# Kernel tuning notes

Measured on AMD Instinct MI355X. Metric: run time of the kernel, lower is better.

## Reference

```python
import jax, jax.numpy as jnp
import numpy as np
from jax import lax

EPS = 1e-5
ODE_T1 = 6.0      # ODEnet uses timestep=6
ODE_NSTEPS = 12   # fixed-step RK4 replacing scipy LSODA


def _gn(x, groups, w, b):
    # GroupNorm over (C//groups, H, W) per group, affine per-channel
    N, C, H, W = x.shape
    xg = x.reshape(N, groups, -1)
    mu = xg.mean(-1, keepdims=True)
    var = xg.var(-1, keepdims=True)
    xn = ((xg - mu) * lax.rsqrt(var + EPS)).reshape(N, C, H, W)
    return xn * w[None, :, None, None] + b[None, :, None, None]


def _conv(x, w, stride=1, pad=1):
    return lax.conv_general_dilated(
        x, w, (stride, stride), [(pad, pad), (pad, pad)],
        dimension_numbers=('NCHW', 'OIHW', 'NCHW'))


def _residual(x, g1w, g1b, c1w, g2w, g2b, c2w, dw):
    # Residual block with stride-2 conv and 1x1 stride-2 downsample applied
    # to relu(norm1(x)) (exactly as in the torch code).
    h = jax.nn.relu(_gn(x, 32, g1w, g1b))
    skip = _conv(h, dw, stride=2, pad=0)
    h = _conv(h, c1w, stride=2, pad=1)
    h = jax.nn.relu(_gn(h, 32, g2w, g2b))
    h = _conv(h, c2w)
    return h + skip


def _odefunc(z, p):
    # ResidualODE.odefunc: GroupNorm with groups == channels (64)
    g1w, g1b, c1w, g2w, g2b, c2w = p
    h = jax.nn.relu(_gn(z, 64, g1w, g1b))
    h = _conv(h, c1w)
    h = jax.nn.relu(_gn(h, 64, g2w, g2b))
    h = _conv(h, c2w)
    return h + z


def _odeint_rk4(z0, p):
    dt = ODE_T1 / ODE_NSTEPS
    def step(z, _):
        k1 = _odefunc(z, p)
        k2 = _odefunc(z + 0.5 * dt * k1, p)
        k3 = _odefunc(z + 0.5 * dt * k2, p)
        k4 = _odefunc(z + dt * k3, p)
        return z + (dt / 6.0) * (k1 + 2.0 * k2 + 2.0 * k3 + k4), None
    z, _ = lax.scan(step, z0, None, length=ODE_NSTEPS)
    return z


def _forward(x, conv1_w, conv1_b,
             r1_g1w, r1_g1b, r1_c1w, r1_g2w, r1_g2b, r1_c2w, r1_dw,
             r2_g1w, r2_g1b, r2_c1w, r2_g2w, r2_g2b, r2_c2w, r2_dw,
             ode_g1w, ode_g1b, ode_c1w, ode_g2w, ode_g2b, ode_c2w,
             fin_gw, fin_gb, fc_w, fc_b):
    out = _conv(x, conv1_w, stride=1, pad=0) + conv1_b[None, :, None, None]  # (B,64,26,26)
    out = _residual(out, r1_g1w, r1_g1b, r1_c1w, r1_g2w, r1_g2b, r1_c2w, r1_dw)  # (B,64,13,13)
    out = _residual(out, r2_g1w, r2_g1b, r2_c1w, r2_g2w, r2_g2b, r2_c2w, r2_dw)  # (B,64,7,7)
    out = _odeint_rk4(out, (ode_g1w, ode_g1b, ode_c1w, ode_g2w, ode_g2b, ode_c2w))
    out = jax.nn.relu(_gn(out, 32, fin_gw, fin_gb))
    out = out.mean(axis=(2, 3))  # AdaptiveAvgPool2d((1,1)) + flatten -> (B,64)
    return out @ fc_w.T + fc_b   # (B,10)


def setup_inputs() -> dict:
    key = jax.random.key(0)
    ks = iter(jax.random.split(key, 16))
    n = lambda shape, s: jax.random.normal(next(ks), shape, dtype=jnp.float32) * s
    C = 64
    s3 = 0.05  # ~ kaiming std for 64x3x3 fan-in
    inp = {
        'x': n((512, 1, 28, 28), 1.0),
        'conv1_w': n((C, 1, 3, 3), 0.3),
        'conv1_b': jnp.zeros((C,), jnp.float32),
        'r1_g1w': jnp.ones((C,), jnp.float32), 'r1_g1b': jnp.zeros((C,), jnp.float32),
        'r1_c1w': n((C, C, 3, 3), s3),
        'r1_g2w': jnp.ones((C,), jnp.float32), 'r1_g2b': jnp.zeros((C,), jnp.float32),
        'r1_c2w': n((C, C, 3, 3), s3),
        'r1_dw': n((C, C, 1, 1), 0.12),
        'r2_g1w': jnp.ones((C,), jnp.float32), 'r2_g1b': jnp.zeros((C,), jnp.float32),
        'r2_c1w': n((C, C, 3, 3), s3),
        'r2_g2w': jnp.ones((C,), jnp.float32), 'r2_g2b': jnp.zeros((C,), jnp.float32),
        'r2_c2w': n((C, C, 3, 3), s3),
        'r2_dw': n((C, C, 1, 1), 0.12),
        'ode_g1w': jnp.ones((C,), jnp.float32), 'ode_g1b': jnp.zeros((C,), jnp.float32),
        'ode_c1w': n((C, C, 3, 3), s3),
        'ode_g2w': jnp.ones((C,), jnp.float32), 'ode_g2b': jnp.zeros((C,), jnp.float32),
        'ode_c2w': n((C, C, 3, 3), s3),
        'fin_gw': jnp.ones((C,), jnp.float32), 'fin_gb': jnp.zeros((C,), jnp.float32),
        'fc_w': n((10, C), 0.1),
        'fc_b': jnp.zeros((10,), jnp.float32),
    }
    return inp


def reference(x, conv1_w, conv1_b,
              r1_g1w, r1_g1b, r1_c1w, r1_g2w, r1_g2b, r1_c2w, r1_dw,
              r2_g1w, r2_g1b, r2_c1w, r2_g2w, r2_g2b, r2_c2w, r2_dw,
              ode_g1w, ode_g1b, ode_c1w, ode_g2w, ode_g2b, ode_c2w,
              fin_gw, fin_gb, fc_w, fc_b):
    return _forward(x, conv1_w, conv1_b,
                    r1_g1w, r1_g1b, r1_c1w, r1_g2w, r1_g2b, r1_c2w, r1_dw,
                    r2_g1w, r2_g1b, r2_c1w, r2_g2w, r2_g2b, r2_c2w, r2_dw,
                    ode_g1w, ode_g1b, ode_c1w, ode_g2w, ode_g2b, ode_c2w,
                    fin_gw, fin_gb, fc_w, fc_b)
```

## Files before the change

### kernel.cpp

```cpp
#include <hip/hip_runtime.h>
#include <hip/hip_bf16.h>

#define TPB 256

typedef __attribute__((ext_vector_type(8))) short short8;
typedef __attribute__((ext_vector_type(4))) float f32x4;

__device__ __forceinline__ unsigned short f2bf(float x) {
    union { float f; unsigned int u; } c; c.f = x;
    unsigned int u = c.u;
    unsigned int r = (u + 0x7fffu + ((u >> 16) & 1u)) >> 16;
    return (unsigned short)r;
}

#define IN_STATS(Xp, HW)                                                        \
    {                                                                           \
        int ch_ = t >> 2, sg_ = t & 3;                                          \
        float s_ = 0.f, s2_ = 0.f;                                              \
        for (int i_ = sg_; i_ < (HW); i_ += 4) {                                \
            float v_ = (Xp)[(size_t)ch_ * (HW) + i_];                           \
            s_ += v_; s2_ += v_ * v_;                                           \
        }                                                                       \
        rsum[t] = s_; rssq[t] = s2_;                                            \
        __syncthreads();                                                        \
        if (t < 32) {                                                           \
            float S = 0.f, S2 = 0.f;                                            \
            _Pragma("unroll")                                                   \
            for (int k_ = 0; k_ < 8; k_++) {                                    \
                int tt_ = (2 * t + (k_ & 1)) * 4 + (k_ >> 1);                   \
                S += rsum[tt_]; S2 += rssq[tt_];                                \
            }                                                                   \
            float mu_ = S / (2.f * (HW));                                       \
            sM[t] = mu_;                                                        \
            sR[t] = rsqrtf(S2 / (2.f * (HW)) - mu_ * mu_ + 1e-5f);              \
        }                                                                       \
        __syncthreads();                                                        \
    }


__global__ void conv1_k(const float* __restrict__ x, const float* __restrict__ w,
                        const float* __restrict__ b, float* __restrict__ out) {
    int idx = blockIdx.x * TPB + threadIdx.x;
    const int total = 512 * 64 * 26 * 26;
    if (idx >= total) return;
    int ox = idx % 26; int t = idx / 26;
    int oy = t % 26;   t /= 26;
    int co = t % 64;   int n = t / 64;
    const float* xp = x + (size_t)n * 784 + oy * 28 + ox;
    const float* wp = w + co * 9;
    float s = b[co];
#pragma unroll
    for (int ky = 0; ky < 3; ky++)
#pragma unroll
        for (int kx = 0; kx < 3; kx++)
            s += xp[ky * 28 + kx] * wp[ky * 3 + kx];
    out[idx] = s;
}


__global__ void gn_stats_k(const float* __restrict__ x, float* __restrict__ mean,
                           float* __restrict__ rstd, int N, int C, int HW, int G) {
    int gid  = (blockIdx.x * blockDim.x + threadIdx.x) >> 6;
    int lane = threadIdx.x & 63;
    int total = N * G;
    if (gid >= total) return;
    int n = gid / G, g = gid % G;
    int cpg = C / G;
    int gsize = cpg * HW;
    const float* p = x + ((size_t)n * C + (size_t)g * cpg) * HW;
    float s = 0.f, s2 = 0.f;
    for (int i = lane; i < gsize; i += 64) { float v = p[i]; s += v; s2 += v * v; }
#pragma unroll
    for (int off = 32; off; off >>= 1) {
        s  += __shfl_down(s,  off);
        s2 += __shfl_down(s2, off);
    }
    if (lane == 0) {
        float m = s / gsize;
        float var = s2 / gsize - m * m;
        mean[gid] = m;
        rstd[gid] = rsqrtf(var + 1e-5f);
    }
}


__global__ void wsplit_all_k(const float* __restrict__ w0, const float* __restrict__ w1,
                             const float* __restrict__ w2, const float* __restrict__ w3,
                             const float* __restrict__ w4, const float* __restrict__ w5,
                             const float* __restrict__ d0, const float* __restrict__ d1,
                             unsigned short* __restrict__ dst) {
    const int WBS = 9 * 2 * 4 * 64 * 8, WBS1 = 2 * 4 * 64 * 8;
    int i = blockIdx.x * TPB + threadIdx.x;
    if (i < 6 * WBS) {
        int tbl = i / WBS; int r = i - tbl * WBS;
        const float* w = (tbl == 0) ? w0 : (tbl == 1) ? w1 : (tbl == 2) ? w2
                       : (tbl == 3) ? w3 : (tbl == 4) ? w4 : w5;
        int j = r & 7, l = (r >> 3) & 63, nt = (r >> 9) & 3, ks = (r >> 11) & 1, tt = r >> 12;
        int co = nt * 16 + (l & 15);
        int ci = ks * 32 + (l >> 4) * 8 + j;
        dst[i] = f2bf(w[(co * 64 + ci) * 9 + tt]);
    } else {
        int r = i - 6 * WBS;
        if (r >= 2 * WBS1) return;
        int tbl = r / WBS1; r -= tbl * WBS1;
        const float* w = tbl ? d1 : d0;
        int j = r & 7, l = (r >> 3) & 63, nt = (r >> 9) & 3, ks = (r >> 11) & 1;
        int co = nt * 16 + (l & 15);
        int ci = ks * 32 + (l >> 4) * 8 + j;
        dst[6 * WBS + tbl * WBS1 + r] = f2bf(w[co * 64 + ci]);
    }
}


template<bool SELF>
__global__ __launch_bounds__(256, 2)
void conv_s2_mfma_k(const float* __restrict__ in,
                    const unsigned short* __restrict__ bhT,
                    const unsigned short* __restrict__ dwT,
                    float* __restrict__ out, float* __restrict__ skipout,
                    const float* __restrict__ mean, const float* __restrict__ rstd,
                    const float* __restrict__ gnw, const float* __restrict__ gnb,
                    int H, int W, int OH, int OW, int TX, int TY) {
    __shared__ unsigned short hp[256 * 72];
    __shared__ float rsum[256], rssq[256], sM[32], sR[32];

    int b = blockIdx.x;
    int tx = b % TX; b /= TX;
    int ty = b % TY; int n = b / TY;
    int oy0 = ty * 7, ox0 = tx * 7;

    const int t = threadIdx.x;
    const int lane = t & 63, nt = t >> 6;
    const int colL = lane & 15, q = lane >> 4;
    const int co = nt * 16 + colL;
    const int kq0 = q * 8;

    short8 wr[18], dr[2];
#pragma unroll
    for (int i = 0; i < 18; i++) wr[i] = ((const short8*)bhT)[(i * 4 + nt) * 64 + lane];
    dr[0] = ((const short8*)dwT)[(0 * 4 + nt) * 64 + lane];
    dr[1] = ((const short8*)dwT)[(1 * 4 + nt) * 64 + lane];

    for (int i = t; i < 256 * 72 / 2; i += 256) ((unsigned int*)hp)[i] = 0u;

    const float* ip = in + (size_t)n * 64 * H * W;
    if constexpr (SELF) {
        IN_STATS(ip, H * W)
    } else {
        if (t < 32) { sM[t] = mean[n * 32 + t]; sR[t] = rstd[n * 32 + t]; }
        __syncthreads();
    }

    for (int i = t; i < 64 * 240; i += 256) {
        int ch = i / 240; int rc = i - ch * 240;
        int r = rc >> 4, c = rc & 15;
        int iy = 2 * oy0 - 1 + r;
        int ix = (c < 8) ? (2 * ox0 + 2 * c) : (2 * ox0 - 1 + 2 * (c - 8));
        if ((unsigned)iy < (unsigned)H && (unsigned)ix < (unsigned)W) {
            float m = sM[ch >> 1], rs = sR[ch >> 1];
            float raw = ip[(size_t)ch * H * W + iy * W + ix];
            float v = fmaxf((raw - m) * rs * gnw[ch] + gnb[ch], 0.f);
            hp[(r * 16 + c) * 72 + ch] = f2bf(v);
        }
    }
    __syncthreads();

    int bs0, bs1, bs2, bs3;
    {
#define BSLOT(dst, mm)                                                          \
        {                                                                       \
            int p_ = (mm) * 16 + colL;                                          \
            int oy_ = p_ >> 3, ox_ = p_ & 7;                                    \
            dst = (ox_ < 7 && oy_ < 7) ? ((2 * oy_) * 16 + ox_) : 0;            \
        }
        BSLOT(bs0, 0) BSLOT(bs1, 1) BSLOT(bs2, 2) BSLOT(bs3, 3)
#undef BSLOT
    }

    f32x4 a0, a1, a2, a3, k0, k1, k2, k3;
    a0 = (f32x4){0.f, 0.f, 0.f, 0.f}; a1 = a0; a2 = a0; a3 = a0;
    k0 = a0; k1 = a0; k2 = a0; k3 = a0;

#pragma unroll
    for (int t9 = 0; t9 < 9; t9++) {
        const int kx = t9 % 3;
        const int toff = (t9 / 3) * 16 + (kx == 0 ? 8 : (kx == 1 ? 0 : 9));
#pragma unroll
        for (int ks = 0; ks < 2; ks++) {
            short8 vb = wr[t9 * 2 + ks];
            int kq = ks * 32 + kq0;
#define TAP(areg, bs)                                                           \
            {                                                                   \
                short8 av = *(const short8*)(hp + ((bs) + toff) * 72 + kq);     \
                areg = __builtin_amdgcn_mfma_f32_16x16x32_bf16(av, vb, areg, 0, 0, 0); \
            }
            TAP(a0, bs0) TAP(a1, bs1) TAP(a2, bs2) TAP(a3, bs3)
#undef TAP
        }
    }
#pragma unroll
    for (int ks = 0; ks < 2; ks++) {
        short8 vb = dr[ks];
        int kq = ks * 32 + kq0;
#define TAP(areg, bs)                                                           \
        {                                                                       \
            short8 av = *(const short8*)(hp + ((bs) + 16) * 72 + kq);           \
            areg = __builtin_amdgcn_mfma_f32_16x16x32_bf16(av, vb, areg, 0, 0, 0); \
        }
        TAP(k0, bs0) TAP(k1, bs1) TAP(k2, bs2) TAP(k3, bs3)
#undef TAP
    }

#define WB(areg, kreg, mm)                                                      \
    _Pragma("unroll")                                                           \
    for (int j = 0; j < 4; j++) {                                               \
        int p_ = (mm) * 16 + q * 4 + j;                                         \
        int oy_ = p_ >> 3, ox_ = p_ & 7;                                        \
        if (ox_ < 7 && oy_ < 7 && oy0 + oy_ < OH && ox0 + ox_ < OW) {           \
            size_t idx = (((size_t)n * 64 + co) * OH + oy0 + oy_) * OW + ox0 + ox_; \
            out[idx] = areg[j];                                                 \
            skipout[idx] = kreg[j];                                             \
        }                                                                       \
    }
    WB(a0, k0, 0) WB(a1, k1, 1) WB(a2, k2, 2) WB(a3, k3, 3)
#undef WB
}


__global__ __launch_bounds__(256, 2)
void conv13_mfma_k(const float* __restrict__ in, const unsigned short* __restrict__ bhT,
                   float* __restrict__ io,
                   const float* __restrict__ gnw, const float* __restrict__ gnb) {
    __shared__ unsigned short hp[256 * 72];
    __shared__ float rsum[256], rssq[256], sM[32], sR[32];
    const int t = threadIdx.x;
    const int n = blockIdx.x;
    const int lane = t & 63;
    const int nt = t >> 6;
    const int colL = lane & 15, q = lane >> 4;
    const int co = nt * 16 + colL;
    const int kq0 = q * 8;

    short8 wr[18];
#pragma unroll
    for (int i = 0; i < 18; i++) wr[i] = ((const short8*)bhT)[(i * 4 + nt) * 64 + lane];

    for (int i = t; i < 256 * 72 / 2; i += 256) ((unsigned int*)hp)[i] = 0u;

    const float* ip = in + (size_t)n * 64 * 169;
    IN_STATS(ip, 169)

    for (int i = t; i < 64 * 169; i += 256) {
        int ch = i / 169, p = i - ch * 169;
        int y = p / 13, x = p - y * 13;
        float m = sM[ch >> 1], rs = sR[ch >> 1];
        float v = fmaxf((ip[i] - m) * rs * gnw[ch] + gnb[ch], 0.f);
        hp[((y + 1) * 16 + (x + 1)) * 72 + ch] = f2bf(v);
    }
    __syncthreads();

    int hb[11];
#pragma unroll
    for (int m = 0; m < 11; m++) {
        int p = m * 16 + colL;
        int y = p / 13, x = p - y * 13;
        hb[m] = (y + 1) * 16 + (x + 1);
    }
    f32x4 acc[11];
#pragma unroll
    for (int m = 0; m < 11; m++) acc[m] = (f32x4){0.f, 0.f, 0.f, 0.f};

#pragma unroll
    for (int t9 = 0; t9 < 9; t9++) {
        const int toff = (t9 / 3) * 16 + (t9 % 3) - 17;
#pragma unroll
        for (int ks = 0; ks < 2; ks++) {
            short8 vb = wr[t9 * 2 + ks];
            int kq = ks * 32 + kq0;
#pragma unroll
            for (int m = 0; m < 11; m++) {
                short8 a_ = *(const short8*)(hp + (hb[m] + toff) * 72 + kq);
                acc[m] = __builtin_amdgcn_mfma_f32_16x16x32_bf16(a_, vb, acc[m], 0, 0, 0);
            }
        }
    }

    float* op = io + (size_t)n * 64 * 169 + (size_t)co * 169;
#pragma unroll
    for (int m = 0; m < 11; m++) {
        int p0 = m * 16 + q * 4;
#pragma unroll
        for (int j = 0; j < 4; j++) {
            int p = p0 + j;
            if (p < 169) op[p] += acc[m][j];
        }
    }
}


#define HP_PITCH 72
#define HP_PLANE (100 * HP_PITCH)

#define PVALID(p) ((((p) & 7) < 7) && (((p) >> 3) < 7))
#define PSLOT(p)  (((((p) >> 3) + 1) * 10) + (((p) & 7) + 1))

#define CONV_TAP(areg, hbase)                                                   \
    {                                                                           \
        short8 a_ = *(const short8*)(hp + ((hbase) + toff) * HP_PITCH + kq);    \
        areg = __builtin_amdgcn_mfma_f32_16x16x32_bf16(a_, vb, areg, 0, 0, 0);  \
    }

#define CONV_MFMA(hpsrc, wreg)                                                  \
    a0 = (f32x4){0.f, 0.f, 0.f, 0.f}; a1 = a0; a2 = a0; a3 = a0;                \
    {                                                                           \
        const unsigned short* hp = (hpsrc);                                     \
        _Pragma("unroll")                                                       \
        for (int t9 = 0; t9 < 9; t9++) {                                        \
            const int toff = (t9 / 3) * 10 + (t9 % 3) - 11;                     \
            _Pragma("unroll")                                                   \
            for (int ks = 0; ks < 2; ks++) {                                    \
                short8 vb = wreg[t9 * 2 + ks];                                  \
                int kq = ks * 32 + kq0;                                         \
                CONV_TAP(a0, h0)                                                \
                CONV_TAP(a1, h1)                                                \
                CONV_TAP(a2, h2)                                                \
                CONV_TAP(a3, h3)                                                \
            }                                                                   \
        }                                                                       \
    }

#define CONV_MFMA_G(hpsrc, bhT)                                                 \
    a0 = (f32x4){0.f, 0.f, 0.f, 0.f}; a1 = a0; a2 = a0; a3 = a0;                \
    {                                                                           \
        const unsigned short* hp = (hpsrc);                                     \
        const short8* bh_ = (const short8*)(bhT);                               \
        _Pragma("unroll")                                                       \
        for (int t9 = 0; t9 < 9; t9++) {                                        \
            const int toff = (t9 / 3) * 10 + (t9 % 3) - 11;                     \
            _Pragma("unroll")                                                   \
            for (int ks = 0; ks < 2; ks++) {                                    \
                short8 vb = bh_[((t9 * 2 + ks) * 4 + nt) * 64 + lane];          \
                int kq = ks * 32 + kq0;                                         \
                CONV_TAP(a0, h0)                                                \
                CONV_TAP(a1, h1)                                                \
                CONV_TAP(a2, h2)                                                \
                CONV_TAP(a3, h3)                                                \
            }                                                                   \
        }                                                                       \
    }

#define GN_ACCUM(areg, mm)                                                      \
    _Pragma("unroll")                                                           \
    for (int j = 0; j < 4; j++) {                                               \
        int p_ = (mm) * 16 + q * 4 + j;                                         \
        if (PVALID(p_)) { float x_ = areg[j]; s += x_; s2 += x_ * x_; }         \
    }

#define GN_STORE(dst, areg, mm)                                                 \
    _Pragma("unroll")                                                           \
    for (int j = 0; j < 4; j++) {                                               \
        int p_ = (mm) * 16 + q * 4 + j;                                         \
        if (PVALID(p_)) {                                                       \
            float y_ = fmaxf(areg[j] * sc + sh, 0.f);                           \
            (dst)[PSLOT(p_) * HP_PITCH + co] = f2bf(y_);                        \
        }                                                                       \
    }

#define RK4_REG(areg, zm, zam, um)                                              \
    {                                                                           \
        f32x4 kv = areg + um;                                                   \
        zam = (e == 0) ? (zm + ck * kv) : (zam + ck * kv);                      \
        if (e < 3) um = zm + cu * kv;                                           \
    }

__global__ __launch_bounds__(256, 2)
void ode_mfma_k(const float* __restrict__ u7raw, const float* __restrict__ z7,
                const float* __restrict__ pgw, const float* __restrict__ pgb,
                const unsigned short* __restrict__ wr2h,
                const unsigned short* __restrict__ wb1h,
                const unsigned short* __restrict__ wb2h,
                const float* __restrict__ g1w, const float* __restrict__ g1b,
                const float* __restrict__ g2w, const float* __restrict__ g2b,
                const float* __restrict__ fgw, const float* __restrict__ fgb,
                const float* __restrict__ fcw, const float* __restrict__ fcb,
                float* __restrict__ out) {
    __shared__ unsigned short hp1[HP_PLANE], hp2[HP_PLANE];
    __shared__ float rsum[256], rssq[256], sM[32], sR[32];
    __shared__ float pooled[64];

    const int t = threadIdx.x;
    const int n = blockIdx.x;
    const int lane = t & 63;
    const int nt = t >> 6;
    const int colL = lane & 15, q = lane >> 4;
    const int co = nt * 16 + colL;

    const float g1wv = g1w[co], g1bv = g1b[co];
    const float g2wv = g2w[co], g2bv = g2b[co];

    const int h0 = PSLOT(colL);
    const int h1 = PSLOT(16 + colL);
    const int h2 = PSLOT(32 + colL);
    const int h3 = PSLOT(48 + colL);
    const int kq0 = q * 8;

    short8 w1r[18], w2r[18];
#pragma unroll
    for (int i = 0; i < 18; i++) {
        int fidx = (i * 4 + nt) * 64 + lane;
        w1r[i] = ((const short8*)wb1h)[fidx];
        w2r[i] = ((const short8*)wb2h)[fidx];
    }

    for (int i = t; i < HP_PLANE; i += 256) { hp1[i] = 0; hp2[i] = 0; }

    const float* up = u7raw + (size_t)n * 3136;
    IN_STATS(up, 49)

    for (int i = t; i < 3136; i += 256) {
        int ch = i / 49, r = i - ch * 49;
        int y = r / 7, x = r - y * 7;
        float m = sM[ch >> 1], rs = sR[ch >> 1];
        float v = fmaxf((up[i] - m) * rs * pgw[ch] + pgb[ch], 0.f);
        hp1[((y + 1) * 10 + (x + 1)) * HP_PITCH + ch] = f2bf(v);
    }
    __syncthreads();

    f32x4 zr0, zr1, zr2, zr3;
    f32x4 za0, za1, za2, za3;
    f32x4 ur0, ur1, ur2, ur3;
    {
        f32x4 a0, a1, a2, a3;
        CONV_MFMA_G(hp1, wr2h)
        const float* zb = z7 + (size_t)n * 3136 + (size_t)co * 49;
#define INITZ(zm, areg, mm)                                                     \
        _Pragma("unroll")                                                       \
        for (int j = 0; j < 4; j++) {                                           \
            int p_ = (mm) * 16 + q * 4 + j;                                     \
            zm[j] = PVALID(p_) ? (areg[j] + zb[(p_ >> 3) * 7 + (p_ & 7)]) : 0.f;\
        }
        INITZ(zr0, a0, 0) INITZ(zr1, a1, 1) INITZ(zr2, a2, 2) INITZ(zr3, a3, 3)
#undef INITZ
    }
    ur0 = zr0; ur1 = zr1; ur2 = zr2; ur3 = zr3;
    __syncthreads();

    const float dt = 0.5f;

#pragma unroll 1
    for (int step = 0; step < 12; step++) {
#pragma unroll 1
        for (int e = 0; e < 4; e++) {
            const float ck = (e == 0 || e == 3) ? dt / 6.f : dt / 3.f;
            const float cu = (e == 2) ? dt : 0.5f * dt;

            {
                float s = 0.f, s2 = 0.f;
                GN_ACCUM(ur0, 0) GN_ACCUM(ur1, 1) GN_ACCUM(ur2, 2) GN_ACCUM(ur3, 3)
                s += __shfl_xor(s, 16); s2 += __shfl_xor(s2, 16);
                s += __shfl_xor(s, 32); s2 += __shfl_xor(s2, 32);
                float mu = s * (1.f / 49.f);
                float r = rsqrtf(s2 * (1.f / 49.f) - mu * mu + 1e-5f);
                float sc = r * g1wv, sh = g1bv - mu * sc;
                GN_STORE(hp1, ur0, 0) GN_STORE(hp1, ur1, 1)
                GN_STORE(hp1, ur2, 2) GN_STORE(hp1, ur3, 3)
            }
            __syncthreads();

            {
                f32x4 a0, a1, a2, a3;
                CONV_MFMA(hp1, w1r)

                float s = 0.f, s2 = 0.f;
                GN_ACCUM(a0, 0) GN_ACCUM(a1, 1) GN_ACCUM(a2, 2) GN_ACCUM(a3, 3)
                s += __shfl_xor(s, 16); s2 += __shfl_xor(s2, 16);
                s += __shfl_xor(s, 32); s2 += __shfl_xor(s2, 32);
                float mu = s * (1.f / 49.f);
                float r = rsqrtf(s2 * (1.f / 49.f) - mu * mu + 1e-5f);
                float sc = r * g2wv, sh = g2bv - mu * sc;
                GN_STORE(hp2, a0, 0) GN_STORE(hp2, a1, 1)
                GN_STORE(hp2, a2, 2) GN_STORE(hp2, a3, 3)
            }
            __syncthreads();

            {
                f32x4 a0, a1, a2, a3;
                CONV_MFMA(hp2, w2r)

                RK4_REG(a0, zr0, za0, ur0) RK4_REG(a1, zr1, za1, ur1)
                RK4_REG(a2, zr2, za2, ur2) RK4_REG(a3, zr3, za3, ur3)
                if (e == 3) {
                    zr0 = za0; zr1 = za1; zr2 = za2; zr3 = za3;
                    ur0 = zr0; ur1 = zr1; ur2 = zr2; ur3 = zr3;
                }
            }
        }
    }

    {
        float s = 0.f, s2 = 0.f;
        GN_ACCUM(zr0, 0) GN_ACCUM(zr1, 1) GN_ACCUM(zr2, 2) GN_ACCUM(zr3, 3)
        s += __shfl_xor(s, 16); s2 += __shfl_xor(s2, 16);
        s += __shfl_xor(s, 32); s2 += __shfl_xor(s2, 32);
        s += __shfl_xor(s, 1);  s2 += __shfl_xor(s2, 1);
        float mu = s * (1.f / 98.f);
        float r = rsqrtf(s2 * (1.f / 98.f) - mu * mu + 1e-5f);
        float sc = r * fgw[co], sh = fgb[co] - mu * sc;
        float ps = 0.f;
#pragma unroll
        for (int mm = 0; mm < 4; mm++) {
            f32x4 zz = (mm == 0) ? zr0 : (mm == 1) ? zr1 : (mm == 2) ? zr2 : zr3;
#pragma unroll
            for (int j = 0; j < 4; j++) {
                int p_ = mm * 16 + q * 4 + j;
                if (PVALID(p_)) ps += fmaxf(zz[j] * sc + sh, 0.f);
            }
        }
        ps += __shfl_xor(ps, 16);
        ps += __shfl_xor(ps, 32);
        if (q == 0) pooled[co] = ps * (1.f / 49.f);
    }
    __syncthreads();
    if (t < 10) {
        float a = fcb[t];
#pragma unroll
        for (int k = 0; k < 64; k++) a += pooled[k] * fcw[t * 64 + k];
        out[(size_t)n * 10 + t] = a;
    }
}

static inline int nblk(long long total) { return (int)((total + TPB - 1) / TPB); }

extern "C" void kernel_launch(void* const* d_in, const int* in_sizes, int n_in,
                              void* d_out, int out_size, void* d_ws, size_t ws_size,
                              hipStream_t stream) {
    const float* x       = (const float*)d_in[0];
    const float* conv1_w = (const float*)d_in[1];
    const float* conv1_b = (const float*)d_in[2];
    const float* r1_g1w  = (const float*)d_in[3];
    const float* r1_g1b  = (const float*)d_in[4];
    const float* r1_c1w  = (const float*)d_in[5];
    const float* r1_g2w  = (const float*)d_in[6];
    const float* r1_g2b  = (const float*)d_in[7];
    const float* r1_c2w  = (const float*)d_in[8];
    const float* r1_dw   = (const float*)d_in[9];
    const float* r2_g1w  = (const float*)d_in[10];
    const float* r2_g1b  = (const float*)d_in[11];
    const float* r2_c1w  = (const float*)d_in[12];
    const float* r2_g2w  = (const float*)d_in[13];
    const float* r2_g2b  = (const float*)d_in[14];
    const float* r2_c2w  = (const float*)d_in[15];
    const float* r2_dw   = (const float*)d_in[16];
    const float* o_g1w   = (const float*)d_in[17];
    const float* o_g1b   = (const float*)d_in[18];
    const float* o_c1w   = (const float*)d_in[19];
    const float* o_g2w   = (const float*)d_in[20];
    const float* o_g2b   = (const float*)d_in[21];
    const float* o_c2w   = (const float*)d_in[22];
    const float* fin_gw  = (const float*)d_in[23];
    const float* fin_gb  = (const float*)d_in[24];
    const float* fc_w    = (const float*)d_in[25];
    const float* fc_b    = (const float*)d_in[26];
    float* out = (float*)d_out;

    const long long SZ26 = 512LL * 64 * 26 * 26;
    const long long SZ13 = 512LL * 64 * 13 * 13;
    const long long SZ7  = 512LL * 64 * 7 * 7;
    const long long WBS  = 9 * 2 * 4 * 64 * 8;
    const long long WBS1 = 2 * 4 * 64 * 8;

    float* B26   = (float*)d_ws;
    float* A13   = B26 + SZ26;
    float* B13   = A13 + SZ13;
    float* Z7    = B13 + SZ13;
    float* U7    = Z7 + SZ7;
    float* MEAN  = U7 + SZ7;
    float* RSTD  = MEAN + 512 * 32;
    unsigned short* WTAB  = (unsigned short*)(RSTD + 512 * 32);
    unsigned short* WB1h  = WTAB;
    unsigned short* WB2h  = WTAB + WBS;
    unsigned short* WB13h = WTAB + 2 * WBS;
    unsigned short* WR2h  = WTAB + 3 * WBS;
    unsigned short* WR11h = WTAB + 4 * WBS;
    unsigned short* WR21h = WTAB + 5 * WBS;
    unsigned short* WD1h  = WTAB + 6 * WBS;
    unsigned short* WD2h  = WTAB + 6 * WBS + WBS1;

    wsplit_all_k<<<nblk(6 * WBS + 2 * WBS1), TPB, 0, stream>>>(
        o_c1w, o_c2w, r1_c2w, r2_c2w, r1_c1w, r2_c1w, r1_dw, r2_dw, WTAB);

    conv1_k<<<nblk(SZ26), TPB, 0, stream>>>(x, conv1_w, conv1_b, B26);

    gn_stats_k<<<nblk(512LL * 32 * 64), TPB, 0, stream>>>(B26, MEAN, RSTD, 512, 64, 676, 32);
    conv_s2_mfma_k<false><<<512 * 4, 256, 0, stream>>>(B26, WR11h, WD1h, A13, B13,
                                                       MEAN, RSTD, r1_g1w, r1_g1b,
                                                       26, 26, 13, 13, 2, 2);
    conv13_mfma_k<<<512, 256, 0, stream>>>(A13, WB13h, B13, r1_g2w, r1_g2b);

    conv_s2_mfma_k<true><<<512, 256, 0, stream>>>(B13, WR21h, WD2h, U7, Z7,
                                                  nullptr, nullptr, r2_g1w, r2_g1b,
                                                  13, 13, 7, 7, 1, 1);

    ode_mfma_k<<<512, 256, 0, stream>>>(U7, Z7, r2_g2w, r2_g2b,
                                        WR2h, WB1h, WB2h,
                                        o_g1w, o_g1b, o_g2w, o_g2b,
                                        fin_gw, fin_gb, fc_w, fc_b, out);
}
```

Measured before the change: 607.5 us.

## Store inter-stage activations in bf16 and raise wave priority during MFMA loops

After: 581.6 us. -4.3%, faster.

```diff
diff --git a/kernel.cpp b/kernel.cpp
--- a/kernel.cpp
+++ b/kernel.cpp
@@ -12,13 +12,17 @@
     unsigned int r = (u + 0x7fffu + ((u >> 16) & 1u)) >> 16;
     return (unsigned short)r;
 }
-
-#define IN_STATS(Xp, HW)                                                        \
+__device__ __forceinline__ float bf2f(unsigned short h) {
+    union { unsigned int u; float f; } c; c.u = ((unsigned int)h) << 16;
+    return c.f;
+}
+
+#define IN_STATS_BF(Xp, HW)                                                     \
     {                                                                           \
         int ch_ = t >> 2, sg_ = t & 3;                                          \
         float s_ = 0.f, s2_ = 0.f;                                              \
         for (int i_ = sg_; i_ < (HW); i_ += 4) {                                \
-            float v_ = (Xp)[(size_t)ch_ * (HW) + i_];                           \
+            float v_ = bf2f((Xp)[(size_t)ch_ * (HW) + i_]);                     \
             s_ += v_; s2_ += v_ * v_;                                           \
         }                                                                       \
         rsum[t] = s_; rssq[t] = s2_;                                            \
@@ -39,7 +43,7 @@
 
 
 __global__ void conv1_k(const float* __restrict__ x, const float* __restrict__ w,
-                        const float* __restrict__ b, float* __restrict__ out) {
+                        const float* __restrict__ b, unsigned short* __restrict__ out) {
     int idx = blockIdx.x * TPB + threadIdx.x;
     const int total = 512 * 64 * 26 * 26;
     if (idx >= total) return;
@@ -54,12 +58,13 @@
 #pragma unroll
         for (int kx = 0; kx < 3; kx++)
             s += xp[ky * 28 + kx] * wp[ky * 3 + kx];
-    out[idx] = s;
-}
-
-
-__global__ void gn_stats_k(const float* __restrict__ x, float* __restrict__ mean,
-                           float* __restrict__ rstd, int N, int C, int HW, int G) {
+    out[idx] = f2bf(s);
+}
+
+
+__global__ void gn_stats_bf_k(const unsigned short* __restrict__ x,
+                              float* __restrict__ mean, float* __restrict__ rstd,
+                              int N, int C, int HW, int G) {
     int gid  = (blockIdx.x * blockDim.x + threadIdx.x) >> 6;
     int lane = threadIdx.x & 63;
     int total = N * G;
@@ -67,9 +72,9 @@
     int n = gid / G, g = gid % G;
     int cpg = C / G;
     int gsize = cpg * HW;
-    const float* p = x + ((size_t)n * C + (size_t)g * cpg) * HW;
+    const unsigned short* p = x + ((size_t)n * C + (size_t)g * cpg) * HW;
     float s = 0.f, s2 = 0.f;
-    for (int i = lane; i < gsize; i += 64) { float v = p[i]; s += v; s2 += v * v; }
+    for (int i = lane; i < gsize; i += 64) { float v = bf2f(p[i]); s += v; s2 += v * v; }
 #pragma unroll
     for (int off = 32; off; off >>= 1) {
         s  += __shfl_down(s,  off);
@@ -112,12 +117,12 @@
 }
 
 
-template<bool SELF>
+template<bool SELF, bool FP32SKIP>
 __global__ __launch_bounds__(256, 2)
-void conv_s2_mfma_k(const float* __restrict__ in,
+void conv_s2_mfma_k(const unsigned short* __restrict__ in,
                     const unsigned short* __restrict__ bhT,
                     const unsigned short* __restrict__ dwT,
-                    float* __restrict__ out, float* __restrict__ skipout,
+                    unsigned short* __restrict__ out, void* __restrict__ skipout_,
                     const float* __restrict__ mean, const float* __restrict__ rstd,
                     const float* __restrict__ gnw, const float* __restrict__ gnb,
                     int H, int W, int OH, int OW, int TX, int TY) {
@@ -143,9 +148,9 @@
 
     for (int i = t; i < 256 * 72 / 2; i += 256) ((unsigned int*)hp)[i] = 0u;
 
-    const float* ip = in + (size_t)n * 64 * H * W;
+    const unsigned short* ip = in + (size_t)n * 64 * H * W;
     if constexpr (SELF) {
-        IN_STATS(ip, H * W)
+        IN_STATS_BF(ip, H * W)
     } else {
         if (t < 32) { sM[t] = mean[n * 32 + t]; sR[t] = rstd[n * 32 + t]; }
         __syncthreads();
@@ -158,7 +163,7 @@
         int ix = (c < 8) ? (2 * ox0 + 2 * c) : (2 * ox0 - 1 + 2 * (c - 8));
         if ((unsigned)iy < (unsigned)H && (unsigned)ix < (unsigned)W) {
             float m = sM[ch >> 1], rs = sR[ch >> 1];
-            float raw = ip[(size_t)ch * H * W + iy * W + ix];
+            float raw = bf2f(ip[(size_t)ch * H * W + iy * W + ix]);
             float v = fmaxf((raw - m) * rs * gnw[ch] + gnb[ch], 0.f);
             hp[(r * 16 + c) * 72 + ch] = f2bf(v);
         }
@@ -218,8 +223,9 @@
         int oy_ = p_ >> 3, ox_ = p_ & 7;                                        \
         if (ox_ < 7 && oy_ < 7 && oy0 + oy_ < OH && ox0 + ox_ < OW) {           \
             size_t idx = (((size_t)n * 64 + co) * OH + oy0 + oy_) * OW + ox0 + ox_; \
-            out[idx] = areg[j];                                                 \
-            skipout[idx] = kreg[j];                                             \
+            out[idx] = f2bf(areg[j]);                                           \
+            if constexpr (FP32SKIP) ((float*)skipout_)[idx] = kreg[j];          \
+            else ((unsigned short*)skipout_)[idx] = f2bf(kreg[j]);              \
         }                                                                       \
     }
     WB(a0, k0, 0) WB(a1, k1, 1) WB(a2, k2, 2) WB(a3, k3, 3)
@@ -228,8 +234,9 @@
 
 
 __global__ __launch_bounds__(256, 2)
-void conv13_mfma_k(const float* __restrict__ in, const unsigned short* __restrict__ bhT,
-                   float* __restrict__ io,
+void conv13_mfma_k(const unsigned short* __restrict__ in,
+                   const unsigned short* __restrict__ bhT,
+                   unsigned short* __restrict__ io,
                    const float* __restrict__ gnw, const float* __restrict__ gnb) {
     __shared__ unsigned short hp[256 * 72];
     __shared__ float rsum[256], rssq[256], sM[32], sR[32];
@@ -247,14 +254,14 @@
 
     for (int i = t; i < 256 * 72 / 2; i += 256) ((unsigned int*)hp)[i] = 0u;
 
-    const float* ip = in + (size_t)n * 64 * 169;
-    IN_STATS(ip, 169)
+    const unsigned short* ip = in + (size_t)n * 64 * 169;
+    IN_STATS_BF(ip, 169)
 
     for (int i = t; i < 64 * 169; i += 256) {
         int ch = i / 169, p = i - ch * 169;
         int y = p / 13, x = p - y * 13;
         float m = sM[ch >> 1], rs = sR[ch >> 1];
-        float v = fmaxf((ip[i] - m) * rs * gnw[ch] + gnb[ch], 0.f);
+        float v = fmaxf((bf2f(ip[i]) - m) * rs * gnw[ch] + gnb[ch], 0.f);
         hp[((y + 1) * 16 + (x + 1)) * 72 + ch] = f2bf(v);
     }
     __syncthreads();
@@ -285,14 +292,14 @@
         }
     }
 
-    float* op = io + (size_t)n * 64 * 169 + (size_t)co * 169;
+    unsigned short* op = io + (size_t)n * 64 * 169 + (size_t)co * 169;
 #pragma unroll
     for (int m = 0; m < 11; m++) {
         int p0 = m * 16 + q * 4;
 #pragma unroll
         for (int j = 0; j < 4; j++) {
             int p = p0 + j;
-            if (p < 169) op[p] += acc[m][j];
+            if (p < 169) op[p] = f2bf(bf2f(op[p]) + acc[m][j]);
         }
     }
 }
@@ -314,6 +321,7 @@
     a0 = (f32x4){0.f, 0.f, 0.f, 0.f}; a1 = a0; a2 = a0; a3 = a0;                \
     {                                                                           \
         const unsigned short* hp = (hpsrc);                                     \
+        __builtin_amdgcn_s_setprio(1);                                          \
         _Pragma("unroll")                                                       \
         for (int t9 = 0; t9 < 9; t9++) {                                        \
             const int toff = (t9 / 3) * 10 + (t9 % 3) - 11;                     \
@@ -327,6 +335,7 @@
                 CONV_TAP(a3, h3)                                                \
             }                                                                   \
         }                                                                       \
+        __builtin_amdgcn_s_setprio(0);                                          \
     }
 
 #define CONV_MFMA_G(hpsrc, bhT)                                                 \
@@ -374,7 +383,7 @@
     }
 
 __global__ __launch_bounds__(256, 2)
-void ode_mfma_k(const float* __restrict__ u7raw, const float* __restrict__ z7,
+void ode_mfma_k(const unsigned short* __restrict__ u7raw, const float* __restrict__ z7,
                 const float* __restrict__ pgw, const float* __restrict__ pgb,
                 const unsigned short* __restrict__ wr2h,
                 const unsigned short* __restrict__ wb1h,
@@ -414,14 +423,14 @@
 
     for (int i = t; i < HP_PLANE; i += 256) { hp1[i] = 0; hp2[i] = 0; }
 
-    const float* up = u7raw + (size_t)n * 3136;
-    IN_STATS(up, 49)
+    const unsigned short* up = u7raw + (size_t)n * 3136;
+    IN_STATS_BF(up, 49)
 
     for (int i = t; i < 3136; i += 256) {
         int ch = i / 49, r = i - ch * 49;
         int y = r / 7, x = r - y * 7;
         float m = sM[ch >> 1], rs = sR[ch >> 1];
-        float v = fmaxf((up[i] - m) * rs * pgw[ch] + pgb[ch], 0.f);
+        float v = fmaxf((bf2f(up[i]) - m) * rs * pgw[ch] + pgb[ch], 0.f);
         hp1[((y + 1) * 10 + (x + 1)) * HP_PITCH + ch] = f2bf(v);
     }
     __syncthreads();
@@ -569,13 +578,13 @@
     const long long WBS  = 9 * 2 * 4 * 64 * 8;
     const long long WBS1 = 2 * 4 * 64 * 8;
 
-    float* B26   = (float*)d_ws;
-    float* A13   = B26 + SZ26;
-    float* B13   = A13 + SZ13;
-    float* Z7    = B13 + SZ13;
-    float* U7    = Z7 + SZ7;
-    float* MEAN  = U7 + SZ7;
-    float* RSTD  = MEAN + 512 * 32;
+    unsigned short* B26 = (unsigned short*)d_ws;
+    unsigned short* A13 = B26 + SZ26;
+    unsigned short* B13 = A13 + SZ13;
+    unsigned short* U7  = B13 + SZ13;
+    float* Z7   = (float*)(U7 + SZ7 + (SZ7 & 1));
+    float* MEAN = Z7 + SZ7;
+    float* RSTD = MEAN + 512 * 32;
     unsigned short* WTAB  = (unsigned short*)(RSTD + 512 * 32);
     unsigned short* WB1h  = WTAB;
     unsigned short* WB2h  = WTAB + WBS;
@@ -591,15 +600,15 @@
 
     conv1_k<<<nblk(SZ26), TPB, 0, stream>>>(x, conv1_w, conv1_b, B26);
 
-    gn_stats_k<<<nblk(512LL * 32 * 64), TPB, 0, stream>>>(B26, MEAN, RSTD, 512, 64, 676, 32);
-    conv_s2_mfma_k<false><<<512 * 4, 256, 0, stream>>>(B26, WR11h, WD1h, A13, B13,
-                                                       MEAN, RSTD, r1_g1w, r1_g1b,
-                                                       26, 26, 13, 13, 2, 2);
+    gn_stats_bf_k<<<nblk(512LL * 32 * 64), TPB, 0, stream>>>(B26, MEAN, RSTD, 512, 64, 676, 32);
+    conv_s2_mfma_k<false, false><<<512 * 4, 256, 0, stream>>>(B26, WR11h, WD1h, A13, B13,
+                                                              MEAN, RSTD, r1_g1w, r1_g1b,
+                                                              26, 26, 13, 13, 2, 2);
     conv13_mfma_k<<<512, 256, 0, stream>>>(A13, WB13h, B13, r1_g2w, r1_g2b);
 
-    conv_s2_mfma_k<true><<<512, 256, 0, stream>>>(B13, WR21h, WD2h, U7, Z7,
-                                                  nullptr, nullptr, r2_g1w, r2_g1b,
-                                                  13, 13, 7, 7, 1, 1);
+    conv_s2_mfma_k<true, true><<<512, 256, 0, stream>>>(B13, WR21h, WD2h, U7, Z7,
+                                                        nullptr, nullptr, r2_g1w, r2_g1b,
+                                                        13, 13, 7, 7, 1, 1);
 
     ode_mfma_k<<<512, 256, 0, stream>>>(U7, Z7, r2_g2w, r2_g2b,
                                         WR2h, WB1h, WB2h,
```
